# Optimization experiments

Measured on AMD Instinct MI355X. Metric: run time of the kernel, lower is better.

The kernel has to match this reference:

```python
import jax, jax.numpy as jnp
import numpy as np

C, FF, NH = 128, 2048, 8
B, D, H, W = 1, 16, 16, 16
EPS = 1e-5

def setup_inputs() -> dict:
    key = jax.random.key(0)
    ks = jax.random.split(key, 20)
    s = 0.02
    inp = {
        'x': jax.random.normal(ks[0], (B, C, D, H, W), jnp.float32),
        'Wq': jax.random.normal(ks[1], (C, C), jnp.float32) * s,
        'bq': jnp.zeros((C,), jnp.float32),
        'Wk': jax.random.normal(ks[2], (C, C), jnp.float32) * s,
        'bk': jnp.zeros((C,), jnp.float32),
        'Wv': jax.random.normal(ks[3], (C, C), jnp.float32) * s,
        'bv': jnp.zeros((C,), jnp.float32),
        'Wo': jax.random.normal(ks[4], (C, C), jnp.float32) * s,
        'bo': jnp.zeros((C,), jnp.float32),
        'W1': jax.random.normal(ks[5], (FF, C), jnp.float32) * s,
        'b1': jnp.zeros((FF,), jnp.float32),
        'W2': jax.random.normal(ks[6], (C, FF), jnp.float32) * s,
        'b2': jnp.zeros((C,), jnp.float32),
        'g1': jnp.ones((C,), jnp.float32),
        'be1': jnp.zeros((C,), jnp.float32),
        'g2': jnp.ones((C,), jnp.float32),
        'be2': jnp.zeros((C,), jnp.float32),
    }
    return inp

def _layernorm(t, g, b):
    # normalize over last (channel) dim, biased variance like torch LayerNorm
    m = jnp.mean(t, axis=-1, keepdims=True)
    v = jnp.mean(jnp.square(t - m), axis=-1, keepdims=True)
    return (t - m) * jax.lax.rsqrt(v + EPS) * g + b

def reference(x, Wq, bq, Wk, bk, Wv, bv, Wo, bo, W1, b1, W2, b2, g1, be1, g2, be2):
    b_, c, d, h, w = x.shape
    n = d * h * w
    hd = c // NH
    xf = x.reshape(b_, c, n)  # [B,C,N]
    # 1x1 conv3d == per-voxel linear over channels
    q = jnp.einsum('oc,bcn->bon', Wq, xf) + bq[:, None]
    k = jnp.einsum('oc,bcn->bon', Wk, xf) + bk[:, None]
    v = jnp.einsum('oc,bcn->bon', Wv, xf) + bv[:, None]
    q = q.reshape(b_, NH, hd, n)
    k = k.reshape(b_, NH, hd, n)
    v = v.reshape(b_, NH, hd, n)
    scores = jnp.einsum('bhcd,bhce->bhde', q, k) / (hd ** 0.5)  # [B,NH,N,N]
    probs = jax.nn.softmax(scores, axis=-1)
    attn = jnp.einsum('bhde,bhce->bhcd', probs, v).reshape(b_, c, n)
    attn = jnp.einsum('oc,bcn->bon', Wo, attn) + bo[:, None]
    x1 = xf + attn  # residual (dropout = identity at eval)
    x1 = _layernorm(x1.transpose(0, 2, 1), g1, be1)  # [B,N,C]
    hmid = jax.nn.relu(jnp.einsum('fc,bnc->bnf', W1, x1) + b1)
    ffn = jnp.einsum('cf,bnf->bnc', W2, hmid) + b2
    x2 = _layernorm(x1 + ffn, g2, be2)
    return x2.transpose(0, 2, 1).reshape(b_, c, d, h, w)
```

## Files before the change

kernel.cpp:

```cpp
#include <hip/hip_runtime.h>
#include <hip/hip_bf16.h>

typedef __hip_bfloat16 bf16;
typedef short short8 __attribute__((ext_vector_type(8)));
typedef float f32x4 __attribute__((ext_vector_type(4)));

#define C_   128
#define N_   4096
#define NH_  8
#define HD_  16
#define FF_  2048
#define SCALE_Q 0.360673760222241f

__device__ __forceinline__ unsigned int pack_trunc(float lo, float hi) {
    return __builtin_amdgcn_perm(__float_as_uint(hi), __float_as_uint(lo), 0x07060302u);
}
__device__ __forceinline__ short f2bf_trunc(float f) {
    return (short)(__float_as_uint(f) >> 16);
}
__device__ __forceinline__ float bfs2f(short s) {
    return __uint_as_float(((unsigned int)(unsigned short)s) << 16);
}
__device__ __forceinline__ float fast_exp2(float x) {
    return __builtin_amdgcn_exp2f(x);
}
__device__ __forceinline__ f32x4 mfma16(short8 a, short8 b, f32x4 c) {
    return __builtin_amdgcn_mfma_f32_16x16x32_bf16(a, b, c, 0, 0, 0);
}
__device__ __forceinline__ int kpos(int ko) { return ((ko & 15) << 1) + (ko >> 4); }

__global__ void k_prep(const float* __restrict__ Wq, const float* __restrict__ Wk,
                       const float* __restrict__ Wv, const float* __restrict__ Wo,
                       const float* __restrict__ W1, const float* __restrict__ W2,
                       const float* __restrict__ x,
                       bf16* __restrict__ Wqkvf, bf16* __restrict__ Wof,
                       bf16* __restrict__ W1f, bf16* __restrict__ W2f,
                       bf16* __restrict__ xTf)
{
    const int i = blockIdx.x * 256 + threadIdx.x;
    if (i < 49152) {
        const int o = i >> 7, k = i & 127;
        const float v = (o < 128) ? Wq[i] : (o < 256) ? Wk[i - 16384] : Wv[i - 32768];
        const int pk = kpos(k & 31);
        Wqkvf[(((o >> 4) << 2) + (k >> 5)) * 512 + (((pk >> 3) << 4) + (o & 15)) * 8 + (pk & 7)]
            = __float2bfloat16(v);
    } else if (i < 65536) {
        const int j = i - 49152, o = j >> 7, k = j & 127;
        const int pk = kpos(k & 31);
        Wof[(((o >> 4) << 2) + (k >> 5)) * 512 + (((pk >> 3) << 4) + (o & 15)) * 8 + (pk & 7)]
            = __float2bfloat16(Wo[j]);
    } else if (i < 327680) {
        const int j = i - 65536, o = j >> 7, k = j & 127;
        const int pk = kpos(k & 31);
        W1f[(((o >> 4) << 2) + (k >> 5)) * 512 + (((pk >> 3) << 4) + (o & 15)) * 8 + (pk & 7)]
            = __float2bfloat16(W1[j]);
    } else if (i < 589824) {
        const int j = i - 327680, o = j >> 11, k = j & 2047;
        const int pk = kpos(k & 31);
        W2f[(((o >> 4) << 6) + (k >> 5)) * 512 + (((pk >> 3) << 4) + (o & 15)) * 8 + (pk & 7)]
            = __float2bfloat16(W2[j]);
    } else if (i < 1114112) {
        const int j = i - 589824, c = j >> 12, n = j & 4095;
        const int pk = kpos(c & 31);
        xTf[(((n >> 4) << 2) + (c >> 5)) * 512 + (((pk >> 3) << 4) + (n & 15)) * 8 + (pk & 7)]
            = __float2bfloat16(x[j]);
    }
}

__global__ void __launch_bounds__(256) k_qkv(
    const bf16* __restrict__ xTf, const bf16* __restrict__ Wqkvf,
    const float* __restrict__ bq, const float* __restrict__ bk, const float* __restrict__ bv,
    bf16* __restrict__ qf, bf16* __restrict__ kf, bf16* __restrict__ vf)
{
    const int tid = threadIdx.x, wave = tid >> 6, lane = tid & 63;
    const int col = lane & 15, quad = lane >> 4;
    const int gw = blockIdx.x * 4 + wave;
    const int rt = gw / 24, ct = gw % 24;
    f32x4 acc = {};
    #pragma unroll
    for (int c = 0; c < 4; ++c) {
        short8 a = *(const short8*)(xTf + ((size_t)(rt * 4 + c) << 9) + lane * 8);
        short8 b = *(const short8*)(Wqkvf + ((size_t)(ct * 4 + c) << 9) + lane * 8);
        acc = mfma16(a, b, acc);
    }
    #pragma unroll
    for (int r = 0; r < 4; ++r) {
        const int m = rt * 16 + quad * 4 + r;
        const int n = ct * 16 + col;
        const float v = acc[r];
        if (n < 128) {
            const int h = n >> 4, ch = n & 15;
            qf[((h << 8) + (m >> 4)) * 256 + (((ch >> 3) << 4) + (m & 15)) * 8 + (ch & 7)] =
                __float2bfloat16((v + bq[n]) * SCALE_Q);
        } else if (n < 256) {
            const int c2 = n - 128, h = c2 >> 4, ch = c2 & 15;
            kf[((h << 8) + (m >> 4)) * 256 + (((ch >> 3) << 4) + (m & 15)) * 8 + (ch & 7)] =
                __float2bfloat16(v + bk[c2]);
        } else {
            const int c2 = n - 256, h = c2 >> 4, ch = c2 & 15;
            const int ko = m & 31;
            const int pos = ((ko & 15) << 1) + (ko >> 4);
            vf[((h << 7) + (m >> 5)) * 512 + (((pos >> 3) << 4) + ch) * 8 + (pos & 7)] =
                __float2bfloat16(v + bv[c2]);
        }
    }
}

__global__ void __launch_bounds__(256)
attn_kernel(const bf16* __restrict__ qf, const bf16* __restrict__ kf,
            const bf16* __restrict__ vf, bf16* __restrict__ af)
{
    __shared__ __align__(16) union {
        unsigned int P[4][2][320];
        float comb[4][64][8];
    } sh;
    const int tid = threadIdx.x, wave = tid >> 6, lane = tid & 63;
    const int col = lane & 15, quad = lane >> 4;
    const int gw = blockIdx.x;
    const int h  = gw >> 8;
    const int tile = gw & 255;
    const f32x4 zero = {};

    short8 aq = {};
    if (quad < 2)
        aq = *(const short8*)(qf + ((size_t)((h << 8) + tile) << 8) + lane * 8);

    const short8 onesb = { (short)0x3F80, (short)0x3F80, (short)0x3F80, (short)0x3F80,
                           (short)0x3F80, (short)0x3F80, (short)0x3F80, (short)0x3F80 };

    f32x4 accO0 = {}, accO1 = {}, accLa = {}, accLb = {};

    const int kbeg = wave << 10;
    unsigned int* P0 = &sh.P[wave][0][0];
    unsigned int* P1 = &sh.P[wave][1][0];

    for (int i = 0; i < 32; i += 2) {
        const int mA = kbeg + (i << 5);
        const int mB = mA + 32;

        short8 bkA0 = {}, bkA1 = {}, bkB0 = {}, bkB1 = {};
        if (quad < 2) {
            const bf16* ka = kf + ((size_t)((h << 8) + (mA >> 4)) << 8) + lane * 8;
            bkA0 = *(const short8*)(ka);
            bkA1 = *(const short8*)(ka + 256);
            bkB0 = *(const short8*)(ka + 512);
            bkB1 = *(const short8*)(ka + 768);
        }
        f32x4 s0 = mfma16(aq, bkA0, zero);
        f32x4 s1 = mfma16(aq, bkA1, zero);
        f32x4 s2 = mfma16(aq, bkB0, zero);
        f32x4 s3 = mfma16(aq, bkB1, zero);
        #pragma unroll
        for (int r = 0; r < 4; ++r) {
            P0[(quad * 4 + r) * 20 + col] = pack_trunc(fast_exp2(s0[r]), fast_exp2(s1[r]));
            P1[(quad * 4 + r) * 20 + col] = pack_trunc(fast_exp2(s2[r]), fast_exp2(s3[r]));
        }
        short8 vA = *(const short8*)(vf + ((size_t)((h << 7) + (mA >> 5)) << 9) + lane * 8);
        short8 vB = *(const short8*)(vf + ((size_t)((h << 7) + (mB >> 5)) << 9) + lane * 8);
        short8 ap0 = *(const short8*)((const short*)P0 + col * 40 + quad * 8);
        accO0 = mfma16(ap0, vA, accO0);
        accLa = mfma16(ap0, onesb, accLa);
        short8 ap1 = *(const short8*)((const short*)P1 + col * 40 + quad * 8);
        accO1 = mfma16(ap1, vB, accO1);
        accLb = mfma16(ap1, onesb, accLb);
    }

    f32x4 accO, accL;
    #pragma unroll
    for (int r = 0; r < 4; ++r) {
        accO[r] = accO0[r] + accO1[r];
        accL[r] = accLa[r] + accLb[r];
    }

    __syncthreads();
    #pragma unroll
    for (int r = 0; r < 4; ++r) {
        sh.comb[wave][lane][r]     = accO[r];
        sh.comb[wave][lane][4 + r] = accL[r];
    }
    __syncthreads();

    if (wave == 0) {
        #pragma unroll
        for (int r = 0; r < 4; ++r) {
            float O = sh.comb[0][lane][r] + sh.comb[1][lane][r]
                    + sh.comb[2][lane][r] + sh.comb[3][lane][r];
            float l = sh.comb[0][lane][4+r] + sh.comb[1][lane][4+r]
                    + sh.comb[2][lane][4+r] + sh.comb[3][lane][4+r];
            const int row16 = quad * 4 + r;
            const int pk = (col << 1) + (h & 1);
            af[((tile << 2) + (h >> 1)) * 512 + (((pk >> 3) << 4) + row16) * 8 + (pk & 7)] =
                __float2bfloat16(O / l);
        }
    }
}

__global__ void __launch_bounds__(256, 1)
k_mega(const bf16* __restrict__ af, const bf16* __restrict__ xTf,
       const bf16* __restrict__ Wof, const bf16* __restrict__ W1f, const bf16* __restrict__ W2f,
       const float* __restrict__ bo, const float* __restrict__ b1, const float* __restrict__ b2,
       const float* __restrict__ g1, const float* __restrict__ be1,
       const float* __restrict__ g2, const float* __restrict__ be2,
       float* __restrict__ out)
{
    __shared__ __align__(16) unsigned int Pb[4][2][320];
    __shared__ float comb[96][64];
    const int tid = threadIdx.x, wave = tid >> 6, lane = tid & 63;
    const int col = lane & 15, quad = lane >> 4;
    const int rt = blockIdx.x, n0 = rt << 4;
    const f32x4 zero = {};

    short8 ao[4], xt[4];
    #pragma unroll
    for (int c = 0; c < 4; ++c) {
        ao[c] = *(const short8*)(af  + ((size_t)(rt * 4 + c) << 9) + lane * 8);
        xt[c] = *(const short8*)(xTf + ((size_t)(rt * 4 + c) << 9) + lane * 8);
    }
    f32x4 d[8];
    #pragma unroll
    for (int t = 0; t < 8; ++t) d[t] = zero;
    #pragma unroll
    for (int t = 0; t < 8; ++t)
        #pragma unroll
        for (int c = 0; c < 4; ++c) {
            short8 b = *(const short8*)(Wof + ((size_t)(t * 4 + c) << 9) + lane * 8);
            d[t] = mfma16(ao[c], b, d[t]);
        }
    #pragma unroll
    for (int t = 0; t < 8; ++t) {
        const float bt = bo[t * 16 + col];
        #pragma unroll
        for (int r = 0; r < 4; ++r) d[t][r] += bt;
    }

    float x1f[4][8];
    #pragma unroll
    for (int c = 0; c < 4; ++c) {
        unsigned int* Pw = &Pb[wave][c & 1][0];
        const short* Ps = (const short*)Pw;
        #pragma unroll
        for (int r = 0; r < 4; ++r)
            Pw[(quad * 4 + r) * 20 + col] = pack_trunc(d[2 * c][r], d[2 * c + 1][r]);
        short8 ar = *(const short8*)(Ps + col * 40 + quad * 8);
        #pragma unroll
        for (int j = 0; j < 8; ++j)
            x1f[c][j] = bfs2f(ar[j]) + bfs2f(xt[c][j]);
    }

    float s = 0.f, ss = 0.f;
    #pragma unroll
    for (int c = 0; c < 4; ++c)
        #pragma unroll
        for (int j = 0; j < 8; ++j) { s += x1f[c][j]; ss += x1f[c][j] * x1f[c][j]; }
    s  += __shfl_xor(s, 16);  s  += __shfl_xor(s, 32);
    ss += __shfl_xor(ss, 16); ss += __shfl_xor(ss, 32);
    const float m1 = s * (1.f / 128.f);
    const float rstd1 = rsqrtf(ss * (1.f / 128.f) - m1 * m1 + 1e-5f);
    short8 aq1[4];
    #pragma unroll
    for (int c = 0; c < 4; ++c)
        #pragma unroll
        for (int j = 0; j < 8; ++j) {
            const int pos = quad * 8 + j;
            const int ko = ((pos & 1) << 4) + (pos >> 1);
            const int ch = c * 32 + ko;
            aq1[c][j] = f2bf_trunc((x1f[c][j] - m1) * rstd1 * g1[ch] + be1[ch]);
        }

    f32x4 ACC[8];
    #pragma unroll
    for (int t = 0; t < 8; ++t) ACC[t] = zero;
    for (int i = 0; i < 16; ++i) {
        const int ffc = (wave << 4) + i;
        f32x4 p0 = zero, p1 = zero;
        #pragma unroll
        for (int c = 0; c < 4; ++c) {
            short8 b = *(const short8*)(W1f + ((size_t)(ffc * 8 + c) << 9) + lane * 8);
            p0 = mfma16(aq1[c], b, p0);
        }
        #pragma unroll
        for (int c = 0; c < 4; ++c) {
            short8 b = *(const short8*)(W1f + ((size_t)(ffc * 8 + 4 + c) << 9) + lane * 8);
            p1 = mfma16(aq1[c], b, p1);
        }
        const float bb0 = b1[ffc * 32 + col], bb1 = b1[ffc * 32 + 16 + col];
        unsigned int* Pw = &Pb[wave][i & 1][0];
        #pragma unroll
        for (int r = 0; r < 4; ++r)
            Pw[(quad * 4 + r) * 20 + col] =
                pack_trunc(fmaxf(p0[r] + bb0, 0.f), fmaxf(p1[r] + bb1, 0.f));
        short8 ah = *(const short8*)((const short*)Pw + col * 40 + quad * 8);
        #pragma unroll
        for (int t = 0; t < 8; ++t) {
            short8 bw = *(const short8*)(W2f + ((size_t)(t * 64 + ffc) << 9) + lane * 8);
            ACC[t] = mfma16(ah, bw, ACC[t]);
        }
    }

    if (wave) {
        #pragma unroll
        for (int t = 0; t < 8; ++t)
            #pragma unroll
            for (int r = 0; r < 4; ++r)
                comb[(wave - 1) * 32 + t * 4 + r][lane] = ACC[t][r];
    }
    __syncthreads();
    if (wave == 0) {
        #pragma unroll
        for (int t = 0; t < 8; ++t)
            #pragma unroll
            for (int r = 0; r < 4; ++r)
                ACC[t][r] += comb[t * 4 + r][lane] + comb[32 + t * 4 + r][lane]
                           + comb[64 + t * 4 + r][lane];
        short* xb = (short*)&Pb[0][0][0];
        #pragma unroll
        for (int c = 0; c < 4; ++c)
            *(short8*)(xb + (col * 4 + c) * 32 + quad * 8) = aq1[c];
        float t2[8][4];
        #pragma unroll
        for (int t = 0; t < 8; ++t) {
            const int ch = t * 16 + col;
            const int pk = (col << 1) + (t & 1);
            const int c = t >> 1;
            const float bb = b2[ch];
            #pragma unroll
            for (int r = 0; r < 4; ++r)
                t2[t][r] = ACC[t][r] + bb + bfs2f(xb[((quad * 4 + r) * 4 + c) * 32 + pk]);
        }
        #pragma unroll
        for (int r = 0; r < 4; ++r) {
            float S = 0.f, SS = 0.f;
            #pragma unroll
            for (int t = 0; t < 8; ++t) { S += t2[t][r]; SS += t2[t][r] * t2[t][r]; }
            S  += __shfl_xor(S, 1);  S  += __shfl_xor(S, 2);
            S  += __shfl_xor(S, 4);  S  += __shfl_xor(S, 8);
            SS += __shfl_xor(SS, 1); SS += __shfl_xor(SS, 2);
            SS += __shfl_xor(SS, 4); SS += __shfl_xor(SS, 8);
            const float m2 = S * (1.f / 128.f);
            const float rstd2 = rsqrtf(SS * (1.f / 128.f) - m2 * m2 + 1e-5f);
            #pragma unroll
            for (int t = 0; t < 8; ++t) {
                const int ch = t * 16 + col;
                out[(size_t)ch * N_ + n0 + quad * 4 + r] =
                    (t2[t][r] - m2) * rstd2 * g2[ch] + be2[ch];
            }
        }
    }
}

extern "C" void kernel_launch(void* const* d_in, const int* in_sizes, int n_in,
                              void* d_out, int out_size, void* d_ws, size_t ws_size,
                              hipStream_t stream) {
    const float* x   = (const float*)d_in[0];
    const float* Wq  = (const float*)d_in[1];
    const float* bq  = (const float*)d_in[2];
    const float* Wk  = (const float*)d_in[3];
    const float* bk  = (const float*)d_in[4];
    const float* Wv  = (const float*)d_in[5];
    const float* bv  = (const float*)d_in[6];
    const float* Wo  = (const float*)d_in[7];
    const float* bo  = (const float*)d_in[8];
    const float* W1  = (const float*)d_in[9];
    const float* b1  = (const float*)d_in[10];
    const float* W2  = (const float*)d_in[11];
    const float* b2  = (const float*)d_in[12];
    const float* g1  = (const float*)d_in[13];
    const float* be1 = (const float*)d_in[14];
    const float* g2  = (const float*)d_in[15];
    const float* be2 = (const float*)d_in[16];
    float* out = (float*)d_out;

    char* ws = (char*)d_ws;
    bf16* xTf   = (bf16*)(ws + 0);
    bf16* qf    = (bf16*)(ws + 1048576);
    bf16* kf    = (bf16*)(ws + 2097152);
    bf16* vf    = (bf16*)(ws + 3145728);
    bf16* af    = (bf16*)(ws + 4194304);
    bf16* Wqkvf = (bf16*)(ws + 5242880);
    bf16* Wof   = (bf16*)(ws + 5341184);
    bf16* W1f   = (bf16*)(ws + 5373952);
    bf16* W2f   = (bf16*)(ws + 5898240);

    k_prep<<<4352, 256, 0, stream>>>(Wq, Wk, Wv, Wo, W1, W2, x, Wqkvf, Wof, W1f, W2f, xTf);
    k_qkv<<<1536, 256, 0, stream>>>(xTf, Wqkvf, bq, bk, bv, qf, kf, vf);
    attn_kernel<<<2048, 256, 0, stream>>>(qf, kf, vf, af);
    k_mega<<<256, 256, 0, stream>>>(af, xTf, Wof, W1f, W2f, bo, b1, b2,
                                    g1, be1, g2, be2, out);
}
```

Measured before the change: 145.2 us.

## Vectorize bf16 weight/input packing and double k_mega waves to eight

k_prep now has each thread convert eight floats and write one 16-byte packed fragment, replacing scalar scattered bf16 stores. This cuts the grid from 4352 to 544 blocks and makes the writes coalesced. k_mega moves to 512 threads, so the FFN loop over FF chunks is split across 8 waves instead of 4, with a larger LDS reduction buffer to combine the partial sums. The extra waves give more parallelism per row tile, at the cost of more shared memory, a longer cross-wave reduction, and tighter register limits under launch bounds (512,2).

Measured after the change: 143.7 us. No clear change (-1.0%).

```diff
diff --git a/kernel.cpp b/kernel.cpp
--- a/kernel.cpp
+++ b/kernel.cpp
@@ -4,6 +4,7 @@
 typedef __hip_bfloat16 bf16;
 typedef short short8 __attribute__((ext_vector_type(8)));
 typedef float f32x4 __attribute__((ext_vector_type(4)));
+typedef unsigned int u32x4 __attribute__((ext_vector_type(4)));
 
 #define C_   128
 #define N_   4096
@@ -12,6 +13,10 @@
 #define FF_  2048
 #define SCALE_Q 0.360673760222241f
 
+__device__ __forceinline__ unsigned short f2bf_bits(float f) {
+    bf16 h = __float2bfloat16(f);
+    return *reinterpret_cast<unsigned short*>(&h);
+}
 __device__ __forceinline__ unsigned int pack_trunc(float lo, float hi) {
     return __builtin_amdgcn_perm(__float_as_uint(hi), __float_as_uint(lo), 0x07060302u);
 }
@@ -27,43 +32,62 @@
 __device__ __forceinline__ f32x4 mfma16(short8 a, short8 b, f32x4 c) {
     return __builtin_amdgcn_mfma_f32_16x16x32_bf16(a, b, c, 0, 0, 0);
 }
-__device__ __forceinline__ int kpos(int ko) { return ((ko & 15) << 1) + (ko >> 4); }
-
-__global__ void k_prep(const float* __restrict__ Wq, const float* __restrict__ Wk,
-                       const float* __restrict__ Wv, const float* __restrict__ Wo,
-                       const float* __restrict__ W1, const float* __restrict__ W2,
-                       const float* __restrict__ x,
-                       bf16* __restrict__ Wqkvf, bf16* __restrict__ Wof,
-                       bf16* __restrict__ W1f, bf16* __restrict__ W2f,
-                       bf16* __restrict__ xTf)
+
+__global__ void __launch_bounds__(256) k_prep(
+    const float* __restrict__ Wq, const float* __restrict__ Wk,
+    const float* __restrict__ Wv, const float* __restrict__ Wo,
+    const float* __restrict__ W1, const float* __restrict__ W2,
+    const float* __restrict__ x,
+    bf16* __restrict__ Wqkvf, bf16* __restrict__ Wof,
+    bf16* __restrict__ W1f, bf16* __restrict__ W2f,
+    bf16* __restrict__ xTf)
 {
     const int i = blockIdx.x * 256 + threadIdx.x;
-    if (i < 49152) {
-        const int o = i >> 7, k = i & 127;
-        const float v = (o < 128) ? Wq[i] : (o < 256) ? Wk[i - 16384] : Wv[i - 32768];
-        const int pk = kpos(k & 31);
-        Wqkvf[(((o >> 4) << 2) + (k >> 5)) * 512 + (((pk >> 3) << 4) + (o & 15)) * 8 + (pk & 7)]
-            = __float2bfloat16(v);
-    } else if (i < 65536) {
-        const int j = i - 49152, o = j >> 7, k = j & 127;
-        const int pk = kpos(k & 31);
-        Wof[(((o >> 4) << 2) + (k >> 5)) * 512 + (((pk >> 3) << 4) + (o & 15)) * 8 + (pk & 7)]
-            = __float2bfloat16(Wo[j]);
-    } else if (i < 327680) {
-        const int j = i - 65536, o = j >> 7, k = j & 127;
-        const int pk = kpos(k & 31);
-        W1f[(((o >> 4) << 2) + (k >> 5)) * 512 + (((pk >> 3) << 4) + (o & 15)) * 8 + (pk & 7)]
-            = __float2bfloat16(W1[j]);
-    } else if (i < 589824) {
-        const int j = i - 327680, o = j >> 11, k = j & 2047;
-        const int pk = kpos(k & 31);
-        W2f[(((o >> 4) << 6) + (k >> 5)) * 512 + (((pk >> 3) << 4) + (o & 15)) * 8 + (pk & 7)]
-            = __float2bfloat16(W2[j]);
-    } else if (i < 1114112) {
-        const int j = i - 589824, c = j >> 12, n = j & 4095;
-        const int pk = kpos(c & 31);
-        xTf[(((n >> 4) << 2) + (c >> 5)) * 512 + (((pk >> 3) << 4) + (n & 15)) * 8 + (pk & 7)]
-            = __float2bfloat16(x[j]);
+    if (i < 73728) {
+        const float* row;
+        bf16* dst;
+        int kblk, g;
+        if (i < 8192) {
+            const int o = i >> 4;
+            kblk = (i >> 2) & 3; g = i & 3;
+            const int odx = (o < 384) ? o : o - 384;
+            row = (o < 128) ? (Wq + o * 128)
+                : (o < 256) ? (Wk + (o - 128) * 128)
+                : (o < 384) ? (Wv + (o - 256) * 128)
+                            : (Wo + (o - 384) * 128);
+            bf16* buf = (o < 384) ? Wqkvf : Wof;
+            dst = buf + ((((odx >> 4) << 2) + kblk) * 512 + ((g << 4) + (odx & 15)) * 8);
+        } else if (i < 40960) {
+            const int t = i - 8192, o = t >> 4;
+            kblk = (t >> 2) & 3; g = t & 3;
+            row = W1 + o * 128;
+            dst = W1f + ((((o >> 4) << 2) + kblk) * 512 + ((g << 4) + (o & 15)) * 8);
+        } else {
+            const int t = i - 40960, o = t >> 8;
+            kblk = (t >> 2) & 63; g = t & 3;
+            row = W2 + o * 2048;
+            dst = W2f + ((((o >> 4) << 6) + kblk) * 512 + ((g << 4) + (o & 15)) * 8);
+        }
+        const int k0 = kblk * 32 + g * 4;
+        const f32x4 lo = *(const f32x4*)(row + k0);
+        const f32x4 hi = *(const f32x4*)(row + k0 + 16);
+        u32x4 w;
+        #pragma unroll
+        for (int j = 0; j < 4; ++j)
+            w[j] = ((unsigned int)f2bf_bits(hi[j]) << 16) | f2bf_bits(lo[j]);
+        *(u32x4*)dst = w;
+    } else {
+        const int t = i - 73728;
+        const int n = t & 4095, g = (t >> 12) & 3, cblk = t >> 14;
+        const int c0 = cblk * 32 + g * 4;
+        const float* xs = x + (size_t)c0 * 4096 + n;
+        u32x4 w;
+        #pragma unroll
+        for (int j = 0; j < 4; ++j)
+            w[j] = ((unsigned int)f2bf_bits(xs[(size_t)(16 + j) * 4096]) << 16)
+                 | f2bf_bits(xs[(size_t)j * 4096]);
+        bf16* dst = xTf + ((((n >> 4) << 2) + cblk) * 512 + ((g << 4) + (n & 15)) * 8);
+        *(u32x4*)dst = w;
     }
 }
 
@@ -195,7 +219,7 @@
     }
 }
 
-__global__ void __launch_bounds__(256, 1)
+__global__ void __launch_bounds__(512, 2)
 k_mega(const bf16* __restrict__ af, const bf16* __restrict__ xTf,
        const bf16* __restrict__ Wof, const bf16* __restrict__ W1f, const bf16* __restrict__ W2f,
        const float* __restrict__ bo, const float* __restrict__ b1, const float* __restrict__ b2,
@@ -203,8 +227,8 @@
        const float* __restrict__ g2, const float* __restrict__ be2,
        float* __restrict__ out)
 {
-    __shared__ __align__(16) unsigned int Pb[4][2][320];
-    __shared__ float comb[96][64];
+    __shared__ __align__(16) unsigned int Pb[8][2][320];
+    __shared__ float comb[224][64];
     const int tid = threadIdx.x, wave = tid >> 6, lane = tid & 63;
     const int col = lane & 15, quad = lane >> 4;
     const int rt = blockIdx.x, n0 = rt << 4;
@@ -270,8 +294,8 @@
     f32x4 ACC[8];
     #pragma unroll
     for (int t = 0; t < 8; ++t) ACC[t] = zero;
-    for (int i = 0; i < 16; ++i) {
-        const int ffc = (wave << 4) + i;
+    for (int i = 0; i < 8; ++i) {
+        const int ffc = (wave << 3) + i;
         f32x4 p0 = zero, p1 = zero;
         #pragma unroll
         for (int c = 0; c < 4; ++c) {
@@ -309,9 +333,13 @@
         #pragma unroll
         for (int t = 0; t < 8; ++t)
             #pragma unroll
-            for (int r = 0; r < 4; ++r)
-                ACC[t][r] += comb[t * 4 + r][lane] + comb[32 + t * 4 + r][lane]
-                           + comb[64 + t * 4 + r][lane];
+            for (int r = 0; r < 4; ++r) {
+                float acc = ACC[t][r];
+                #pragma unroll
+                for (int w = 0; w < 7; ++w)
+                    acc += comb[w * 32 + t * 4 + r][lane];
+                ACC[t][r] = acc;
+            }
         short* xb = (short*)&Pb[0][0][0];
         #pragma unroll
         for (int c = 0; c < 4; ++c)
@@ -381,9 +409,9 @@
     bf16* W1f   = (bf16*)(ws + 5373952);
     bf16* W2f   = (bf16*)(ws + 5898240);
 
-    k_prep<<<4352, 256, 0, stream>>>(Wq, Wk, Wv, Wo, W1, W2, x, Wqkvf, Wof, W1f, W2f, xTf);
+    k_prep<<<544, 256, 0, stream>>>(Wq, Wk, Wv, Wo, W1, W2, x, Wqkvf, Wof, W1f, W2f, xTf);
     k_qkv<<<1536, 256, 0, stream>>>(xTf, Wqkvf, bq, bk, bv, qf, kf, vf);
     attn_kernel<<<2048, 256, 0, stream>>>(qf, kf, vf, af);
-    k_mega<<<256, 256, 0, stream>>>(af, xTf, Wof, W1f, W2f, bo, b1, b2,
+    k_mega<<<256, 512, 0, stream>>>(af, xTf, Wof, W1f, W2f, bo, b1, b2,
                                     g1, be1, g2, be2, out);
 }
```
